# Optimization experiments

Hardware: AMD Instinct MI355X
Metric: run time of the kernel (lower is better)

## Reference

```python
import jax, jax.numpy as jnp
import numpy as np

BETA = 0.25
N_E = 8192
E_DIM = 64
B, L = 32, 512


def setup_inputs() -> dict:
    key = jax.random.key(0)
    k1, k2, k3 = jax.random.split(key, 3)
    z = jax.random.normal(k1, (B, E_DIM, L), dtype=jnp.float32)
    mask = jax.random.randint(k2, (B, L), 0, 2, dtype=jnp.int32)
    # nn.Embedding init: uniform(-1/n_e, 1/n_e)
    emb = jax.random.uniform(k3, (N_E, E_DIM), dtype=jnp.float32,
                             minval=-1.0 / N_E, maxval=1.0 / N_E)
    return {"z": z, "mask": mask, "emb": emb}


def reference(z, mask, emb):
    sg = jax.lax.stop_gradient
    b, c, l = z.shape            # c == e_dim
    n_e = emb.shape[0]
    zt = jnp.transpose(z, (0, 2, 1))          # (B, L, C)
    zf = zt.reshape(-1, c)                    # (B*L, C)
    m = mask.reshape(-1, 1).astype(zf.dtype)  # (B*L, 1) per-token mask

    # pairwise squared distances (with masked z, as in original)
    zm = zf * m
    d = (jnp.sum(zf * zf * m, axis=1, keepdims=True)
         + jnp.sum(emb * emb, axis=1)
         - 2.0 * jnp.matmul(zm, emb.T))       # (B*L, n_e)

    idx = jnp.argmin(d, axis=1)               # (B*L,)
    min_encodings = jax.nn.one_hot(idx, n_e, dtype=zf.dtype)  # (B*L, n_e)
    z_q = emb[idx].reshape(zt.shape)          # gather == one_hot @ emb

    # masked MSE losses (mask broadcast over the C dim, mean over mask.sum()*C)
    m3 = m.reshape(b, l, 1)
    denom = jnp.sum(m3) * c
    embedding_loss = jnp.sum((sg(z_q) - zt) ** 2 * m3) / denom
    commitment_loss = jnp.sum((z_q - sg(zt)) ** 2 * m3) / denom
    loss = embedding_loss + BETA * commitment_loss

    # straight-through estimator
    z_q_st = zt + sg(z_q - zt)

    e_mean = jnp.mean(min_encodings, axis=0)
    perplexity = jnp.exp(-jnp.sum(e_mean * jnp.log(e_mean + 1e-10)))

    z_q_out = jnp.transpose(z_q_st, (0, 2, 1))  # back to (B, C, L)
    return loss, z_q_out, perplexity, min_encodings, idx[:, None]
```

## Files before the change

kernel.cpp:

```cpp
#include <hip/hip_runtime.h>
#include <cstdint>
#include <cstddef>

#define TOK 16384
#define NE  8192
#define CD  64

#define O_ZQ   1
#define O_PERP 1048577
#define O_ENC  1048578
#define O_IDX  135266306

__global__ __launch_bounds__(256) void k_init(
    const float* __restrict__ z, const int* __restrict__ mask,
    const float* __restrict__ emb,
    unsigned long long* __restrict__ packed,
    float* __restrict__ s_z, float* __restrict__ s_e,
    int* __restrict__ hist) {
  int g = blockIdx.x * 256 + threadIdx.x;
  if (g < TOK) {
    int t = g, b = t >> 9, l = t & 511;
    const float* zp = z + (size_t)b * 32768 + l;
    float r[8];
#pragma unroll
    for (int j = 0; j < 8; ++j) { float v = zp[(size_t)j * 512]; r[j] = __fmul_rn(v, v); }
#pragma unroll
    for (int i = 8; i < 64; i += 8)
#pragma unroll
      for (int j = 0; j < 8; ++j) { float v = zp[(size_t)(i + j) * 512]; r[j] = __fadd_rn(r[j], __fmul_rn(v, v)); }
    float s = __fadd_rn(__fadd_rn(__fadd_rn(r[0], r[1]), __fadd_rn(r[2], r[3])),
                        __fadd_rn(__fadd_rn(r[4], r[5]), __fadd_rn(r[6], r[7])));
    s_z[t] = mask[t] ? s : 0.0f;
    packed[t] = ~0ull;
  } else if (g < TOK + NE) {
    int i = g - TOK;
    const float* ep = emb + (size_t)i * 64;
    float r[8];
#pragma unroll
    for (int j = 0; j < 8; ++j) { float v = ep[j]; r[j] = __fmul_rn(v, v); }
#pragma unroll
    for (int kk = 8; kk < 64; kk += 8)
#pragma unroll
      for (int j = 0; j < 8; ++j) { float v = ep[kk + j]; r[j] = __fadd_rn(r[j], __fmul_rn(v, v)); }
    float s = __fadd_rn(__fadd_rn(__fadd_rn(r[0], r[1]), __fadd_rn(r[2], r[3])),
                        __fadd_rn(__fadd_rn(r[4], r[5]), __fadd_rn(r[6], r[7])));
    s_e[i] = s;
    hist[i] = 0;
  }
}

__global__ __launch_bounds__(256) void k_search(
    const float* __restrict__ z, const int* __restrict__ mask,
    const float* __restrict__ emb,
    const float* __restrict__ s_z, const float* __restrict__ s_e,
    unsigned long long* __restrict__ packed,
    float* __restrict__ enc_out) {
  __shared__ __align__(16) float zs[64][68];
  __shared__ __align__(16) float es[128][68];

  const int tid = threadIdx.x;
  const int I0 = blockIdx.x * 128;
  const int T0 = blockIdx.y * 64;
  const int b  = T0 >> 9;
  const int l0 = T0 & 511;

  {
    int lq = tid & 63;
    int m  = mask[T0 + lq];
#pragma unroll
    for (int rep = 0; rep < 16; ++rep) {
      int c = (tid >> 6) + rep * 4;
      float v = z[(size_t)b * 32768 + (size_t)c * 512 + l0 + lq];
      zs[lq][c] = m ? v : 0.0f;
    }
  }
  {
    int cq = tid & 63;
#pragma unroll
    for (int rep = 0; rep < 32; ++rep) {
      int i = (tid >> 6) + rep * 4;
      es[i][cq] = emb[(size_t)(I0 + i) * 64 + cq];
    }
  }
  __syncthreads();

  {
    const float4 z4 = make_float4(0.f, 0.f, 0.f, 0.f);
    float* base = enc_out + (size_t)T0 * 8192 + I0;
#pragma unroll
    for (int r = 0; r < 8; ++r) {
      int id  = r * 256 + tid;
      int row = id >> 5;
      int c4  = id & 31;
      *(float4*)(base + (size_t)row * 8192 + c4 * 4) = z4;
    }
  }

  const int ty = tid >> 4;
  const int tx = tid & 15;

  float szv[4], sev[8];
#pragma unroll
  for (int m = 0; m < 4; ++m) szv[m] = s_z[T0 + ty * 4 + m];
#pragma unroll
  for (int j = 0; j < 8; ++j) sev[j] = s_e[I0 + tx + 16 * j];

  float acc[4][8];
#pragma unroll
  for (int m = 0; m < 4; ++m)
#pragma unroll
    for (int j = 0; j < 8; ++j) acc[m][j] = 0.0f;

#pragma unroll 2
  for (int k = 0; k < 64; k += 4) {
    float4 zv[4], ev[8];
#pragma unroll
    for (int m = 0; m < 4; ++m) zv[m] = *(const float4*)&zs[ty * 4 + m][k];
#pragma unroll
    for (int j = 0; j < 8; ++j) ev[j] = *(const float4*)&es[tx + 16 * j][k];
#pragma unroll
    for (int m = 0; m < 4; ++m)
#pragma unroll
      for (int j = 0; j < 8; ++j) {
        acc[m][j] = fmaf(zv[m].x, ev[j].x, acc[m][j]);
        acc[m][j] = fmaf(zv[m].y, ev[j].y, acc[m][j]);
        acc[m][j] = fmaf(zv[m].z, ev[j].z, acc[m][j]);
        acc[m][j] = fmaf(zv[m].w, ev[j].w, acc[m][j]);
      }
  }

  unsigned long long best[4] = {~0ull, ~0ull, ~0ull, ~0ull};
#pragma unroll
  for (int j = 0; j < 8; ++j) {
    int i = I0 + tx + 16 * j;
#pragma unroll
    for (int m = 0; m < 4; ++m) {
      float c1 = __fadd_rn(szv[m], sev[j]);
      float d  = __fsub_rn(c1, __fmul_rn(2.0f, acc[m][j]));
      unsigned int db = __float_as_uint(d);
      db = ((int)db < 0) ? ~db : (db | 0x80000000u);
      unsigned long long p = ((unsigned long long)db << 32) | (unsigned int)i;
      best[m] = (p < best[m]) ? p : best[m];
    }
  }

  __syncthreads();
  unsigned long long* red = reinterpret_cast<unsigned long long*>(&zs[0][0]);
#pragma unroll
  for (int m = 0; m < 4; ++m) red[(ty * 4 + m) * 16 + tx] = best[m];
  __syncthreads();

  if (tid < 64) {
    unsigned long long bb = red[tid * 16];
#pragma unroll
    for (int x = 1; x < 16; ++x) {
      unsigned long long q = red[tid * 16 + x];
      bb = (q < bb) ? q : bb;
    }
    atomicMin(&packed[T0 + tid], bb);
  }
}

__global__ __launch_bounds__(512) void k_finalize(
    const float* __restrict__ z, const int* __restrict__ mask,
    const float* __restrict__ emb,
    const unsigned long long* __restrict__ packed,
    float* __restrict__ out_zq, float* __restrict__ out_enc,
    float* __restrict__ out_idx,
    int* __restrict__ hist, float* __restrict__ token_loss) {
  __shared__ float part[8][64];
  const int T0   = blockIdx.x * 64;
  const int lane = threadIdx.x & 63;
  const int w    = threadIdx.x >> 6;
  const int b    = T0 >> 9;
  const int l0   = T0 & 511;
  const int t    = T0 + lane;

  const int idx = (int)(unsigned int)(packed[t] & 0xFFFFFFFFu);

  const float* zb = z      + (size_t)b * 32768 + l0 + lane;
  float*       qb = out_zq + (size_t)b * 32768 + l0 + lane;

  float sq = 0.0f;
#pragma unroll
  for (int cc = 0; cc < 8; ++cc) {
    int c = w * 8 + cc;
    float zv   = zb[(size_t)c * 512];
    float e    = emb[(size_t)idx * 64 + c];
    float diff = __fsub_rn(e, zv);
    qb[(size_t)c * 512] = __fadd_rn(zv, diff);
    sq = fmaf(diff, diff, sq);
  }
  part[w][lane] = sq;
  __syncthreads();

  if (w == 0) {
    float s = __fadd_rn(
        __fadd_rn(__fadd_rn(part[0][lane], part[1][lane]),
                  __fadd_rn(part[2][lane], part[3][lane])),
        __fadd_rn(__fadd_rn(part[4][lane], part[5][lane]),
                  __fadd_rn(part[6][lane], part[7][lane])));
    token_loss[t] = mask[t] ? s : 0.0f;
    out_idx[t] = (float)idx;
    out_enc[(size_t)t * 8192 + idx] = 1.0f;
    atomicAdd(&hist[idx], 1);
  }
}

__global__ __launch_bounds__(256) void k_scalars(
    const float* __restrict__ token_loss, const int* __restrict__ mask,
    const int* __restrict__ hist, float* __restrict__ out) {
  __shared__ float sf[256];
  __shared__ int   si[256];
  __shared__ float sh[256];
  int tid = threadIdx.x;
  float s = 0.f, h = 0.f;
  int ms = 0;
  for (int i = tid; i < TOK; i += 256) { s += token_loss[i]; ms += mask[i]; }
  for (int i = tid; i < NE; i += 256) {
    float pm = (float)hist[i] * (1.0f / 16384.0f);
    h += pm * logf(pm + 1e-10f);
  }
  sf[tid] = s; si[tid] = ms; sh[tid] = h;
  __syncthreads();
  for (int off = 128; off; off >>= 1) {
    if (tid < off) { sf[tid] += sf[tid + off]; si[tid] += si[tid + off]; sh[tid] += sh[tid + off]; }
    __syncthreads();
  }
  if (tid == 0) {
    float denom = (float)(si[0] * 64);
    float el = sf[0] / denom;
    out[0]      = __fadd_rn(el, __fmul_rn(0.25f, el));
    out[O_PERP] = expf(-sh[0]);
  }
}

extern "C" void kernel_launch(void* const* d_in, const int* in_sizes, int n_in,
                              void* d_out, int out_size, void* d_ws, size_t ws_size,
                              hipStream_t stream) {
  const float* z    = (const float*)d_in[0];
  const int*   mask = (const int*)d_in[1];
  const float* emb  = (const float*)d_in[2];
  float* out = (float*)d_out;
  char*  ws  = (char*)d_ws;

  unsigned long long* packed = (unsigned long long*)ws;
  float* s_z        = (float*)(ws + 131072);
  float* s_e        = (float*)(ws + 196608);
  int*   hist       = (int*)  (ws + 229376);
  float* token_loss = (float*)(ws + 262144);

  k_init<<<96, 256, 0, stream>>>(z, mask, emb, packed, s_z, s_e, hist);

  dim3 g1(64, 256, 1);
  k_search<<<g1, 256, 0, stream>>>(z, mask, emb, s_z, s_e, packed, out + O_ENC);

  k_finalize<<<256, 512, 0, stream>>>(z, mask, emb, packed,
                                      out + O_ZQ, out + O_ENC, out + O_IDX,
                                      hist, token_loss);

  k_scalars<<<1, 256, 0, stream>>>(token_loss, mask, hist, out);
}
```

Before: 385.1 us.

## Hold each token's z in registers and stream codebook rows in search kernel

The search kernel is restructured so each thread keeps one token's 64-dim z vector in registers and loops over 512 codebook rows, which are read uniformly from global memory, instead of a shared-memory tiled 64x128 GEMM. The per-token norm now lives inside the search kernel, so k_init no longer computes it. The zeroing of the one-hot output is interleaved with the search loop. The single-block scalar reduction is split into a 64-block partial kernel plus a small final kernel. The new inner loop uses scalar uniform loads and a single accumulator per thread, which can lose the register-level reuse of the old tile and may be compute-latency bound.

New measurement: 510.0 us. 32.4% more time.

```diff
diff --git a/kernel.cpp b/kernel.cpp
--- a/kernel.cpp
+++ b/kernel.cpp
@@ -4,7 +4,6 @@
 
 #define TOK 16384
 #define NE  8192
-#define CD  64
 
 #define O_ZQ   1
 #define O_PERP 1048577
@@ -12,29 +11,12 @@
 #define O_IDX  135266306
 
 __global__ __launch_bounds__(256) void k_init(
-    const float* __restrict__ z, const int* __restrict__ mask,
     const float* __restrict__ emb,
     unsigned long long* __restrict__ packed,
-    float* __restrict__ s_z, float* __restrict__ s_e,
-    int* __restrict__ hist) {
+    float* __restrict__ s_e, int* __restrict__ hist) {
   int g = blockIdx.x * 256 + threadIdx.x;
-  if (g < TOK) {
-    int t = g, b = t >> 9, l = t & 511;
-    const float* zp = z + (size_t)b * 32768 + l;
-    float r[8];
-#pragma unroll
-    for (int j = 0; j < 8; ++j) { float v = zp[(size_t)j * 512]; r[j] = __fmul_rn(v, v); }
-#pragma unroll
-    for (int i = 8; i < 64; i += 8)
-#pragma unroll
-      for (int j = 0; j < 8; ++j) { float v = zp[(size_t)(i + j) * 512]; r[j] = __fadd_rn(r[j], __fmul_rn(v, v)); }
-    float s = __fadd_rn(__fadd_rn(__fadd_rn(r[0], r[1]), __fadd_rn(r[2], r[3])),
-                        __fadd_rn(__fadd_rn(r[4], r[5]), __fadd_rn(r[6], r[7])));
-    s_z[t] = mask[t] ? s : 0.0f;
-    packed[t] = ~0ull;
-  } else if (g < TOK + NE) {
-    int i = g - TOK;
-    const float* ep = emb + (size_t)i * 64;
+  if (g < NE) {
+    const float* ep = emb + (size_t)g * 64;
     float r[8];
 #pragma unroll
     for (int j = 0; j < 8; ++j) { float v = ep[j]; r[j] = __fmul_rn(v, v); }
@@ -44,121 +26,73 @@
       for (int j = 0; j < 8; ++j) { float v = ep[kk + j]; r[j] = __fadd_rn(r[j], __fmul_rn(v, v)); }
     float s = __fadd_rn(__fadd_rn(__fadd_rn(r[0], r[1]), __fadd_rn(r[2], r[3])),
                         __fadd_rn(__fadd_rn(r[4], r[5]), __fadd_rn(r[6], r[7])));
-    s_e[i] = s;
-    hist[i] = 0;
-  }
+    s_e[g] = s;
+    hist[g] = 0;
+  }
+  packed[g] = ~0ull;
 }
 
 __global__ __launch_bounds__(256) void k_search(
     const float* __restrict__ z, const int* __restrict__ mask,
-    const float* __restrict__ emb,
-    const float* __restrict__ s_z, const float* __restrict__ s_e,
+    const float* __restrict__ emb, const float* __restrict__ s_e,
     unsigned long long* __restrict__ packed,
     float* __restrict__ enc_out) {
-  __shared__ __align__(16) float zs[64][68];
-  __shared__ __align__(16) float es[128][68];
-
-  const int tid = threadIdx.x;
-  const int I0 = blockIdx.x * 128;
-  const int T0 = blockIdx.y * 64;
-  const int b  = T0 >> 9;
-  const int l0 = T0 & 511;
-
-  {
-    int lq = tid & 63;
-    int m  = mask[T0 + lq];
-#pragma unroll
-    for (int rep = 0; rep < 16; ++rep) {
-      int c = (tid >> 6) + rep * 4;
-      float v = z[(size_t)b * 32768 + (size_t)c * 512 + l0 + lq];
-      zs[lq][c] = m ? v : 0.0f;
+  const int tid  = threadIdx.x;
+  const int lane = tid & 63;
+  const int w    = tid >> 6;
+  const int T0   = blockIdx.x * 256;
+  const int I0   = blockIdx.y * 512;
+  const int t    = T0 + w * 64 + lane;
+  const int b    = t >> 9;
+  const int l    = t & 511;
+
+  const int m = mask[t];
+  const float* zb = z + (size_t)b * 32768 + l;
+  float zr[64];
+#pragma unroll
+  for (int c = 0; c < 64; ++c) {
+    float v = zb[(size_t)c * 512];
+    zr[c] = m ? v : 0.0f;
+  }
+
+  float rr[8];
+#pragma unroll
+  for (int j = 0; j < 8; ++j) rr[j] = __fmul_rn(zr[j], zr[j]);
+#pragma unroll
+  for (int i = 8; i < 64; i += 8)
+#pragma unroll
+    for (int j = 0; j < 8; ++j) rr[j] = __fadd_rn(rr[j], __fmul_rn(zr[i + j], zr[i + j]));
+  const float sz = __fadd_rn(__fadd_rn(__fadd_rn(rr[0], rr[1]), __fadd_rn(rr[2], rr[3])),
+                             __fadd_rn(__fadd_rn(rr[4], rr[5]), __fadd_rn(rr[6], rr[7])));
+
+  float* encb = enc_out + (size_t)T0 * 8192 + I0;
+  const float4 zero4 = make_float4(0.f, 0.f, 0.f, 0.f);
+
+  unsigned long long best = ~0ull;
+
+  for (int ii = 0; ii < 512; ++ii) {
+    const int i = I0 + ii;
+    const float se = s_e[i];
+    const float* ep = emb + (size_t)i * 64;
+    float acc = 0.0f;
+#pragma unroll
+    for (int k = 0; k < 64; ++k) acc = fmaf(ep[k], zr[k], acc);
+
+    float d = __fsub_rn(__fadd_rn(sz, se), __fmul_rn(2.0f, acc));
+    unsigned int db = __float_as_uint(d);
+    db = ((int)db < 0) ? ~db : (db | 0x80000000u);
+    unsigned long long p = ((unsigned long long)db << 32) | (unsigned int)i;
+    best = (p < best) ? p : best;
+
+    if ((ii & 3) == 0) {
+      int id  = (ii >> 2) * 256 + tid;
+      int row = id >> 7;
+      int c4  = id & 127;
+      *(float4*)(encb + (size_t)row * 8192 + c4 * 4) = zero4;
     }
   }
-  {
-    int cq = tid & 63;
-#pragma unroll
-    for (int rep = 0; rep < 32; ++rep) {
-      int i = (tid >> 6) + rep * 4;
-      es[i][cq] = emb[(size_t)(I0 + i) * 64 + cq];
-    }
-  }
-  __syncthreads();
-
-  {
-    const float4 z4 = make_float4(0.f, 0.f, 0.f, 0.f);
-    float* base = enc_out + (size_t)T0 * 8192 + I0;
-#pragma unroll
-    for (int r = 0; r < 8; ++r) {
-      int id  = r * 256 + tid;
-      int row = id >> 5;
-      int c4  = id & 31;
-      *(float4*)(base + (size_t)row * 8192 + c4 * 4) = z4;
-    }
-  }
-
-  const int ty = tid >> 4;
-  const int tx = tid & 15;
-
-  float szv[4], sev[8];
-#pragma unroll
-  for (int m = 0; m < 4; ++m) szv[m] = s_z[T0 + ty * 4 + m];
-#pragma unroll
-  for (int j = 0; j < 8; ++j) sev[j] = s_e[I0 + tx + 16 * j];
-
-  float acc[4][8];
-#pragma unroll
-  for (int m = 0; m < 4; ++m)
-#pragma unroll
-    for (int j = 0; j < 8; ++j) acc[m][j] = 0.0f;
-
-#pragma unroll 2
-  for (int k = 0; k < 64; k += 4) {
-    float4 zv[4], ev[8];
-#pragma unroll
-    for (int m = 0; m < 4; ++m) zv[m] = *(const float4*)&zs[ty * 4 + m][k];
-#pragma unroll
-    for (int j = 0; j < 8; ++j) ev[j] = *(const float4*)&es[tx + 16 * j][k];
-#pragma unroll
-    for (int m = 0; m < 4; ++m)
-#pragma unroll
-      for (int j = 0; j < 8; ++j) {
-        acc[m][j] = fmaf(zv[m].x, ev[j].x, acc[m][j]);
-        acc[m][j] = fmaf(zv[m].y, ev[j].y, acc[m][j]);
-        acc[m][j] = fmaf(zv[m].z, ev[j].z, acc[m][j]);
-        acc[m][j] = fmaf(zv[m].w, ev[j].w, acc[m][j]);
-      }
-  }
-
-  unsigned long long best[4] = {~0ull, ~0ull, ~0ull, ~0ull};
-#pragma unroll
-  for (int j = 0; j < 8; ++j) {
-    int i = I0 + tx + 16 * j;
-#pragma unroll
-    for (int m = 0; m < 4; ++m) {
-      float c1 = __fadd_rn(szv[m], sev[j]);
-      float d  = __fsub_rn(c1, __fmul_rn(2.0f, acc[m][j]));
-      unsigned int db = __float_as_uint(d);
-      db = ((int)db < 0) ? ~db : (db | 0x80000000u);
-      unsigned long long p = ((unsigned long long)db << 32) | (unsigned int)i;
-      best[m] = (p < best[m]) ? p : best[m];
-    }
-  }
-
-  __syncthreads();
-  unsigned long long* red = reinterpret_cast<unsigned long long*>(&zs[0][0]);
-#pragma unroll
-  for (int m = 0; m < 4; ++m) red[(ty * 4 + m) * 16 + tx] = best[m];
-  __syncthreads();
-
-  if (tid < 64) {
-    unsigned long long bb = red[tid * 16];
-#pragma unroll
-    for (int x = 1; x < 16; ++x) {
-      unsigned long long q = red[tid * 16 + x];
-      bb = (q < bb) ? q : bb;
-    }
-    atomicMin(&packed[T0 + tid], bb);
-  }
+
+  atomicMin(&packed[t], best);
 }
 
 __global__ __launch_bounds__(512) void k_finalize(
@@ -207,31 +141,47 @@
   }
 }
 
-__global__ __launch_bounds__(256) void k_scalars(
+__global__ __launch_bounds__(256) void k_partial(
     const float* __restrict__ token_loss, const int* __restrict__ mask,
-    const int* __restrict__ hist, float* __restrict__ out) {
-  __shared__ float sf[256];
-  __shared__ int   si[256];
-  __shared__ float sh[256];
-  int tid = threadIdx.x;
-  float s = 0.f, h = 0.f;
-  int ms = 0;
-  for (int i = tid; i < TOK; i += 256) { s += token_loss[i]; ms += mask[i]; }
-  for (int i = tid; i < NE; i += 256) {
-    float pm = (float)hist[i] * (1.0f / 16384.0f);
-    h += pm * logf(pm + 1e-10f);
-  }
-  sf[tid] = s; si[tid] = ms; sh[tid] = h;
+    const int* __restrict__ hist, float* __restrict__ partials) {
+  __shared__ float sf[256], sm[256], sh[256];
+  const int bb = blockIdx.x, tid = threadIdx.x;
+  int ti = bb * 256 + tid;
+  sf[tid] = token_loss[ti];
+  sm[tid] = (float)mask[ti];
+  float h = 0.f;
+  if (tid < 128) {
+    float pm = (float)hist[bb * 128 + tid] * (1.0f / 16384.0f);
+    h = pm * logf(pm + 1e-10f);
+  }
+  sh[tid] = h;
   __syncthreads();
   for (int off = 128; off; off >>= 1) {
-    if (tid < off) { sf[tid] += sf[tid + off]; si[tid] += si[tid + off]; sh[tid] += sh[tid + off]; }
+    if (tid < off) { sf[tid] += sf[tid + off]; sm[tid] += sm[tid + off]; sh[tid] += sh[tid + off]; }
     __syncthreads();
   }
   if (tid == 0) {
-    float denom = (float)(si[0] * 64);
-    float el = sf[0] / denom;
+    partials[bb]       = sf[0];
+    partials[64 + bb]  = sm[0];
+    partials[128 + bb] = sh[0];
+  }
+}
+
+__global__ __launch_bounds__(64) void k_final(
+    const float* __restrict__ partials, float* __restrict__ out) {
+  int tn = threadIdx.x;
+  float lo = partials[tn], mc = partials[64 + tn], en = partials[128 + tn];
+#pragma unroll
+  for (int off = 32; off; off >>= 1) {
+    lo += __shfl_down(lo, off, 64);
+    mc += __shfl_down(mc, off, 64);
+    en += __shfl_down(en, off, 64);
+  }
+  if (tn == 0) {
+    float denom = mc * 64.0f;
+    float el = lo / denom;
     out[0]      = __fadd_rn(el, __fmul_rn(0.25f, el));
-    out[O_PERP] = expf(-sh[0]);
+    out[O_PERP] = expf(-en);
   }
 }
 
@@ -245,19 +195,20 @@
   char*  ws  = (char*)d_ws;
 
   unsigned long long* packed = (unsigned long long*)ws;
-  float* s_z        = (float*)(ws + 131072);
-  float* s_e        = (float*)(ws + 196608);
-  int*   hist       = (int*)  (ws + 229376);
-  float* token_loss = (float*)(ws + 262144);
-
-  k_init<<<96, 256, 0, stream>>>(z, mask, emb, packed, s_z, s_e, hist);
-
-  dim3 g1(64, 256, 1);
-  k_search<<<g1, 256, 0, stream>>>(z, mask, emb, s_z, s_e, packed, out + O_ENC);
+  float* s_e        = (float*)(ws + 131072);
+  int*   hist       = (int*)  (ws + 163840);
+  float* token_loss = (float*)(ws + 196608);
+  float* partials   = (float*)(ws + 262144);
+
+  k_init<<<64, 256, 0, stream>>>(emb, packed, s_e, hist);
+
+  dim3 g1(64, 16, 1);
+  k_search<<<g1, 256, 0, stream>>>(z, mask, emb, s_e, packed, out + O_ENC);
 
   k_finalize<<<256, 512, 0, stream>>>(z, mask, emb, packed,
                                       out + O_ZQ, out + O_ENC, out + O_IDX,
                                       hist, token_loss);
 
-  k_scalars<<<1, 256, 0, stream>>>(token_loss, mask, hist, out);
-}
+  k_partial<<<64, 256, 0, stream>>>(token_loss, mask, hist, partials);
+  k_final<<<1, 64, 0, stream>>>(partials, out);
+}
```
